# Kernel optimization log

Hardware: AMD Instinct MI355X
Metric: run time of the kernel (lower is better)

## Reference

```python
import jax, jax.numpy as jnp
import numpy as np

N, E, IN, ED, H, C = 50000, 800000, 128, 32, 4, 32
HC = H * C
SCALE = 1.0 / float(np.sqrt(C))


def _seg_softmax(t, idx, n):
    # t: [E, H], idx: [E] target-node ids -> per-segment softmax over incoming edges
    m = jax.ops.segment_max(t, idx, num_segments=n)
    m = jnp.where(jnp.isfinite(m), m, 0.0)
    e = jnp.exp(t - m[idx])
    z = jax.ops.segment_sum(e, idx, num_segments=n)
    return e / (z[idx] + 1e-16)


def setup_inputs() -> dict:
    key = jax.random.key(0)
    ks = jax.random.split(key, 26)
    w = lambda k, shape: (jax.random.normal(k, shape, jnp.float32) * 0.05)
    return {
        "x": jax.random.normal(ks[0], (N, IN), jnp.float32),
        "edge_index": jax.random.randint(ks[1], (2, E), 0, N),
        "edge_attr": jax.random.normal(ks[2], (E, ED), jnp.float32),
        # DifferentialGraphAttention params (dual QK groups + lambda)
        "Wq1": w(ks[3], (HC, IN)), "Wq2": w(ks[4], (HC, IN)),
        "Wk1": w(ks[5], (HC, IN)), "Wk2": w(ks[6], (HC, IN)),
        "Wvd": w(ks[7], (HC, IN)),
        "Wkr1": w(ks[8], (HC, ED)), "Wkr2": w(ks[9], (HC, ED)),
        "Wvrd": w(ks[10], (HC, ED)),
        "Woutd": w(ks[11], (HC, HC)),
        "lam": jnp.float32(0.8),
        # RelationActivationAttention params
        "Wqa": w(ks[12], (HC, IN)), "Wka": w(ks[13], (HC, IN)), "Wva": w(ks[14], (HC, IN)),
        "Wkra": w(ks[15], (HC, ED)), "Wvra": w(ks[16], (HC, ED)),
        "Wouta": w(ks[17], (HC, HC)),
        # Hybrid fusion params
        "Wproj": w(ks[18], (HC, 2 * HC)), "bproj": jnp.zeros((HC,), jnp.float32),
        "Win": w(ks[19], (HC, IN)), "b_in": jnp.zeros((HC,), jnp.float32),
        "rms_w": jnp.ones((HC,), jnp.float32),
    }


def reference(x, edge_index, edge_attr, Wq1, Wq2, Wk1, Wk2, Wvd, Wkr1, Wkr2, Wvrd,
              Woutd, lam, Wqa, Wka, Wva, Wkra, Wvra, Wouta, Wproj, bproj, Win, b_in,
              rms_w):
    src, dst = edge_index[0], edge_index[1]

    def nproj(W):  # [N, HC] -> [N, H, C]
        return (x @ W.T).reshape(N, H, C)

    def eproj(W):  # [E, HC] -> [E, H, C]
        return (edge_attr @ W.T).reshape(E, H, C)

    # ---- differential relation aggregation branch ----
    Q1, Q2, K1, K2, Vd = nproj(Wq1), nproj(Wq2), nproj(Wk1), nproj(Wk2), nproj(Wvd)
    t1 = jnp.sum(Q1[dst] * (K1[src] + eproj(Wkr1)), axis=-1) * SCALE  # [E, H]
    t2 = jnp.sum(Q2[dst] * (K2[src] + eproj(Wkr2)), axis=-1) * SCALE
    a_diff = _seg_softmax(t1, dst, N) - lam * _seg_softmax(t2, dst, N)
    msg_d = (Vd[src] + eproj(Wvrd)) * a_diff[..., None]               # [E, H, C]
    h_aggr = jax.ops.segment_sum(msg_d, dst, num_segments=N).reshape(N, HC) @ Woutd.T

    # ---- relation activation branch ----
    Qa, Ka, Va = nproj(Wqa), nproj(Wka), nproj(Wva)
    ta = jnp.sum(Qa[dst] * (Ka[src] + eproj(Wkra)), axis=-1) * SCALE  # [E, H]
    a_act = _seg_softmax(ta, dst, N)
    msg_a = (Va[src] + eproj(Wvra)) * a_act[..., None]
    h_actv = jax.ops.segment_sum(msg_a, dst, num_segments=N).reshape(N, HC) @ Wouta.T

    # ---- hybrid fusion + residual + RMSNorm ----
    h = jnp.concatenate([h_aggr, h_actv], axis=-1) @ Wproj.T + bproj
    h = h + (x @ Win.T + b_in)
    h = h * jax.lax.rsqrt(jnp.mean(h * h, axis=-1, keepdims=True) + 1e-6) * rms_w
    return h
```

## Files before the change

### kernel.cpp

```cpp
#include <hip/hip_runtime.h>

typedef unsigned short u16;
typedef unsigned int   u32;
typedef _Float16 half8 __attribute__((ext_vector_type(8)));
typedef _Float16 half2v __attribute__((ext_vector_type(2)));
typedef float    f32x4 __attribute__((ext_vector_type(4)));

#define NN 50000
#define EE 800000
#define SCALE 0.17677669529663687f
#define NB 49

#define O_WNODET   0ul
#define O_WFT      393216ul
#define O_WF1      524288ul
#define O_WF3      589824ul
#define O_HIST     655360ul
#define O_BSUM     855360ul
#define O_BOFF     855616ul
#define O_OFF      856064ul
#define O_CUR      1056768ul
#define O_PERM     1257472ul
#define O_NODEF    7657472ul
#define O_G        161257472ul

__device__ __forceinline__ float fin(float x){
  return (x == x && fabsf(x) < 3e38f) ? x : 0.f;
}
__device__ __forceinline__ u32 packh(float a, float b){
  union{ u32 u; _Float16 h[2]; } cv; cv.h[0]=(_Float16)a; cv.h[1]=(_Float16)b; return cv.u;
}
union H2U { u32 u; half2v h; };
__device__ __forceinline__ half2v h2(u32 u){ H2U c; c.u=u; return c.h; }
__device__ __forceinline__ u32 u2(half2v h){ H2U c; c.h=h; return c.u; }

__global__ __launch_bounds__(256) void prep1(
    const float* __restrict__ Wq1, const float* __restrict__ Wq2, const float* __restrict__ Wqa,
    const float* __restrict__ Wk1, const float* __restrict__ Wk2, const float* __restrict__ Wka,
    const float* __restrict__ Wvd, const float* __restrict__ Wva, const float* __restrict__ Win,
    const float* __restrict__ Wkr1, const float* __restrict__ Wkr2, const float* __restrict__ Wkra,
    const float* __restrict__ Wproj, const float* __restrict__ Woutd, const float* __restrict__ Wouta,
    _Float16* __restrict__ WnodeT, float* __restrict__ Wf1, float* __restrict__ Wf3)
{
  int job = blockIdx.x*256 + threadIdx.x;
  if (job < 1536*128) {
    int n = job >> 7, kk = job & 127;
    int slot = n >> 7, o = n & 127;
    float val;
    if (slot==3 || slot==4 || slot==5) {
      const float* Wkr = (slot==3)?Wkr1:(slot==4)?Wkr2:Wkra;
      const float* Wq  = (slot==3)?Wq1 :(slot==4)?Wq2 :Wqa;
      int h=o>>5, j=o&31;
      float s=0.f;
      for (int c=0;c<32;c++)
        s += Wkr[(h*32+c)*32 + j] * Wq[(h*32+c)*128 + kk];
      val = s;
    } else {
      const float* W = (slot==0)?Wq1:(slot==1)?Wq2:(slot==2)?Wqa:
                       (slot==6)?Wk1:(slot==7)?Wk2:(slot==8)?Wka:
                       (slot==9)?Wvd:(slot==10)?Wva:Win;
      val = W[o*128 + kk];
    }
    WnodeT[n*128 + kk] = (_Float16)fin(val);
  } else {
    int idx = job - 1536*128;
    int which = idx >> 14;
    int r = idx & 16383;
    int o = r >> 7, v = r & 127;
    const float* Wout = which ? Wouta : Woutd;
    float s=0.f;
    for (int u=0;u<128;u++)
      s += Wproj[o*256 + which*128 + u] * Wout[u*128 + v];
    (which?Wf3:Wf1)[o*128+v] = fin(s);
  }
}

__global__ __launch_bounds__(256) void prep2(
    const float* __restrict__ Wf1, const float* __restrict__ Wf3,
    const float* __restrict__ Wvrd, const float* __restrict__ Wvra,
    _Float16* __restrict__ WfT)
{
  int job = blockIdx.x*256 + threadIdx.x;
  int o = job >> 9, kk = job & 511;
  int seg = kk >> 7, v = kk & 127;
  float val;
  if (seg==0) val = Wf1[o*128+v];
  else if (seg==2) val = Wf3[o*128+v];
  else {
    const float* Wf = (seg==1)?Wf1:Wf3;
    const float* Wv = (seg==1)?Wvrd:Wvra;
    int h=v>>5, j=v&31; float s=0.f;
    for (int c=0;c<32;c++)
      s += Wf[o*128 + h*32 + c] * Wv[(h*32+c)*32 + j];
    val = s;
  }
  WfT[o*512 + kk] = (_Float16)fin(val);
}

__global__ __launch_bounds__(256) void gemm_node(
    const float* __restrict__ x, const _Float16* __restrict__ WnodeT,
    const float* __restrict__ b_in, _Float16* __restrict__ nodeF)
{
  __shared__ _Float16 As[128][72];
  __shared__ _Float16 Bs[128][72];
  int m0 = blockIdx.x * 128;
  int n0 = blockIdx.y * 128;
  int tid = threadIdx.x;
  int lane = tid & 63, wave = tid >> 6;
  int lm = lane & 15, lq = lane >> 4;
  int mbase = wave*32;
  f32x4 acc[2][8];
  #pragma unroll
  for (int i=0;i<2;i++)
    #pragma unroll
    for (int j=0;j<8;j++) acc[i][j] = (f32x4){0.f,0.f,0.f,0.f};

  for (int kt=0; kt<2; kt++){
    int kk0 = kt*64;
    #pragma unroll
    for (int i=0;i<4;i++){
      int c = tid + i*256;
      int row = c >> 3, kc = (c & 7) * 8;
      int grow = m0 + row;
      half8 hv;
      if (grow < NN){
        float4 v0 = *(const float4*)(x + (size_t)grow*128 + kk0 + kc);
        float4 v1 = *(const float4*)(x + (size_t)grow*128 + kk0 + kc + 4);
        hv[0]=(_Float16)v0.x; hv[1]=(_Float16)v0.y; hv[2]=(_Float16)v0.z; hv[3]=(_Float16)v0.w;
        hv[4]=(_Float16)v1.x; hv[5]=(_Float16)v1.y; hv[6]=(_Float16)v1.z; hv[7]=(_Float16)v1.w;
      } else {
        #pragma unroll
        for (int j=0;j<8;j++) hv[j] = (_Float16)0.f;
      }
      *(half8*)&As[row][kc] = hv;
      *(half8*)&Bs[row][kc] = *(const half8*)(WnodeT + (size_t)(n0+row)*128 + kk0 + kc);
    }
    __syncthreads();
    #pragma unroll
    for (int ks=0; ks<64; ks+=32){
      half8 a0 = *(half8*)&As[mbase + lm][ks + lq*8];
      half8 a1 = *(half8*)&As[mbase + 16 + lm][ks + lq*8];
      #pragma unroll
      for (int ct=0; ct<8; ct++){
        half8 b = *(half8*)&Bs[ct*16 + lm][ks + lq*8];
        acc[0][ct] = __builtin_amdgcn_mfma_f32_16x16x32_f16(a0, b, acc[0][ct], 0,0,0);
        acc[1][ct] = __builtin_amdgcn_mfma_f32_16x16x32_f16(a1, b, acc[1][ct], 0,0,0);
      }
    }
    __syncthreads();
  }
  #pragma unroll
  for (int rt=0; rt<2; rt++){
    #pragma unroll
    for (int reg=0; reg<4; reg++){
      int row = m0 + mbase + rt*16 + lq*4 + reg;
      if (row < NN){
        #pragma unroll
        for (int ct=0; ct<8; ct++){
          int colg = n0 + ct*16 + lm;
          float bias = (colg >= 1408) ? b_in[colg-1408] : 0.f;
          nodeF[(size_t)row*1536 + colg] = (_Float16)fin(acc[rt][ct][reg] + bias);
        }
      }
    }
  }
}

__global__ __launch_bounds__(256) void hist_k(const int* __restrict__ ei, int* __restrict__ hist){
  int e = blockIdx.x*256 + threadIdx.x;
  int d = ei[EE + e];
  if ((unsigned)d < (unsigned)NN) atomicAdd(&hist[d], 1);
}

__global__ __launch_bounds__(1024) void scan1(const int* __restrict__ hist,
                                              int* __restrict__ loc, int* __restrict__ bsum){
  __shared__ int buf[1024];
  int i = blockIdx.x*1024 + threadIdx.x;
  int v = (i < NN) ? hist[i] : 0;
  buf[threadIdx.x] = v;
  __syncthreads();
  int xv = v;
  for (int s = 1; s < 1024; s <<= 1){
    int t = 0;
    if ((int)threadIdx.x >= s) t = buf[threadIdx.x - s];
    __syncthreads();
    xv += t;
    buf[threadIdx.x] = xv;
    __syncthreads();
  }
  if (i < NN) loc[i] = xv - v;
  if (threadIdx.x == 1023) bsum[blockIdx.x] = xv;
}

__global__ __launch_bounds__(64) void scan2(const int* __restrict__ bsum, int* __restrict__ boff){
  int t = threadIdx.x;
  int v = (t < NB) ? bsum[t] : 0;
  int x = v;
  for (int s = 1; s < 64; s <<= 1){
    int u = __shfl_up(x, s);
    if (t >= s) x += u;
  }
  if (t < NB) boff[t] = x - v;
}

__global__ __launch_bounds__(256) void scatter_k(const int* __restrict__ ei,
                                                 const int* __restrict__ loc, const int* __restrict__ boff,
                                                 int* __restrict__ cur, int2* __restrict__ pe2){
  int e = blockIdx.x*256 + threadIdx.x;
  int d = ei[EE + e];
  if ((unsigned)d >= (unsigned)NN) return;
  int pos = loc[d] + boff[d>>10] + atomicAdd(&cur[d], 1);
  if ((unsigned)pos < (unsigned)EE) pe2[pos] = make_int2(e, ei[e]);
}

__global__ __launch_bounds__(256) void attn_k(
    const int2* __restrict__ pe2, const int* __restrict__ hist,
    const int* __restrict__ loc, const int* __restrict__ boff,
    const u32* __restrict__ nf, const float4* __restrict__ ea4,
    const float* __restrict__ lamp, u32* __restrict__ G)
{
  int lane = threadIdx.x & 63, wave = threadIdx.x >> 6;
  int node = blockIdx.x*4 + wave;
  if (node >= NN) return;
  int E = lane >> 4;
  int l = lane & 15;
  int h = l >> 2;
  u32 bd = (u32)node * 768u;
  const u32* pd = nf + bd;

  H2U q1[4], q2[4], qa[4], r1[4], r2[4], ra[4];
  {
    uint4 a = *(const uint4*)(pd +        l*4);
    uint4 b = *(const uint4*)(pd +  64 + l*4);
    uint4 c = *(const uint4*)(pd + 128 + l*4);
    q1[0].u=a.x; q1[1].u=a.y; q1[2].u=a.z; q1[3].u=a.w;
    q2[0].u=b.x; q2[1].u=b.y; q2[2].u=b.z; q2[3].u=b.w;
    qa[0].u=c.x; qa[1].u=c.y; qa[2].u=c.z; qa[3].u=c.w;
    int rb = h*16 + (l&3)*4;
    uint4 d = *(const uint4*)(pd + 192 + rb);
    uint4 e = *(const uint4*)(pd + 256 + rb);
    uint4 f = *(const uint4*)(pd + 320 + rb);
    r1[0].u=d.x; r1[1].u=d.y; r1[2].u=d.z; r1[3].u=d.w;
    r2[0].u=e.x; r2[1].u=e.y; r2[2].u=e.z; r2[3].u=e.w;
    ra[0].u=f.x; ra[1].u=f.y; ra[2].u=f.z; ra[3].u=f.w;
  }

  int k = hist[node];
  if (k < 0) k = 0;
  if (k > 64) k = 64;
  int o = loc[node] + boff[node>>10];
  if (o < 0) o = 0;

  H2U s1v[4], s2v[4], sav[4], s1e[4], s2e[4], sae[4];
  #pragma unroll
  for (int t=0;t<4;t++){ s1v[t].u=0; s2v[t].u=0; sav[t].u=0; s1e[t].u=0; s2e[t].u=0; sae[t].u=0; }
  float z1=0.f, z2=0.f, za=0.f;

  int iters = (k + 3) >> 2;
  for (int it=0; it<iters; it++){
    int ei = it*4 + E;
    bool valid = ei < k;
    int ci = valid ? ei : (k-1);
    int2 es = pe2[o + ci];
    int sn = es.y; if ((unsigned)sn >= (unsigned)NN) sn = 0;
    int ee = es.x; if ((unsigned)ee >= (unsigned)EE) ee = 0;
    const u32* ps = nf + (u32)sn * 768u + (u32)(l*4);
    uint4 K1 = *(const uint4*)(ps + 384);
    uint4 K2 = *(const uint4*)(ps + 448);
    uint4 KA = *(const uint4*)(ps + 512);
    uint4 VD = *(const uint4*)(ps + 576);
    uint4 VA = *(const uint4*)(ps + 640);
    float4 ef0 = ea4[(size_t)ee*8 + (l&3)*2];
    float4 ef1 = ea4[(size_t)ee*8 + (l&3)*2 + 1];
    half2v e0 = {(_Float16)ef0.x, (_Float16)ef0.y};
    half2v e1 = {(_Float16)ef0.z, (_Float16)ef0.w};
    half2v e2 = {(_Float16)ef1.x, (_Float16)ef1.y};
    half2v e3 = {(_Float16)ef1.z, (_Float16)ef1.w};

    half2v p1h = q1[0].h*h2(K1.x) + q1[1].h*h2(K1.y) + q1[2].h*h2(K1.z) + q1[3].h*h2(K1.w)
               + r1[0].h*e0 + r1[1].h*e1 + r1[2].h*e2 + r1[3].h*e3;
    half2v p2h = q2[0].h*h2(K2.x) + q2[1].h*h2(K2.y) + q2[2].h*h2(K2.z) + q2[3].h*h2(K2.w)
               + r2[0].h*e0 + r2[1].h*e1 + r2[2].h*e2 + r2[3].h*e3;
    half2v pah = qa[0].h*h2(KA.x) + qa[1].h*h2(KA.y) + qa[2].h*h2(KA.z) + qa[3].h*h2(KA.w)
               + ra[0].h*e0 + ra[1].h*e1 + ra[2].h*e2 + ra[3].h*e3;

    H2U c1, c2, c3, t;
    c1.h = p1h; c2.h = p2h; c3.h = pah;
    t.u = __shfl_xor(c1.u, 1); c1.h += t.h;
    t.u = __shfl_xor(c2.u, 1); c2.h += t.h;
    t.u = __shfl_xor(c3.u, 1); c3.h += t.h;
    t.u = __shfl_xor(c1.u, 2); c1.h += t.h;
    t.u = __shfl_xor(c2.u, 2); c2.h += t.h;
    t.u = __shfl_xor(c3.u, 2); c3.h += t.h;
    float p1 = (float)c1.h[0] + (float)c1.h[1];
    float p2 = (float)c2.h[0] + (float)c2.h[1];
    float pa = (float)c3.h[0] + (float)c3.h[1];

    float w1 = valid ? __expf(p1*SCALE) : 0.f;
    float w2 = valid ? __expf(p2*SCALE) : 0.f;
    float wa = valid ? __expf(pa*SCALE) : 0.f;
    _Float16 w1f = (_Float16)w1, w2f = (_Float16)w2, waf = (_Float16)wa;
    half2v w1h = {w1f, w1f}, w2h = {w2f, w2f}, wah = {waf, waf};

    s1v[0].h += w1h*h2(VD.x); s1v[1].h += w1h*h2(VD.y); s1v[2].h += w1h*h2(VD.z); s1v[3].h += w1h*h2(VD.w);
    s2v[0].h += w2h*h2(VD.x); s2v[1].h += w2h*h2(VD.y); s2v[2].h += w2h*h2(VD.z); s2v[3].h += w2h*h2(VD.w);
    sav[0].h += wah*h2(VA.x); sav[1].h += wah*h2(VA.y); sav[2].h += wah*h2(VA.z); sav[3].h += wah*h2(VA.w);
    s1e[0].h += w1h*e0; s1e[1].h += w1h*e1; s1e[2].h += w1h*e2; s1e[3].h += w1h*e3;
    s2e[0].h += w2h*e0; s2e[1].h += w2h*e1; s2e[2].h += w2h*e2; s2e[3].h += w2h*e3;
    sae[0].h += wah*e0; sae[1].h += wah*e1; sae[2].h += wah*e2; sae[3].h += wah*e3;
    z1 += w1; z2 += w2; za += wa;
  }

  #pragma unroll
  for (int s=16; s<=32; s<<=1){
    H2U t;
    #pragma unroll
    for (int j=0;j<4;j++){
      t.u = __shfl_xor(s1v[j].u, s); s1v[j].h += t.h;
      t.u = __shfl_xor(s2v[j].u, s); s2v[j].h += t.h;
      t.u = __shfl_xor(sav[j].u, s); sav[j].h += t.h;
      t.u = __shfl_xor(s1e[j].u, s); s1e[j].h += t.h;
      t.u = __shfl_xor(s2e[j].u, s); s2e[j].h += t.h;
      t.u = __shfl_xor(sae[j].u, s); sae[j].h += t.h;
    }
    z1 += __shfl_xor(z1, s); z2 += __shfl_xor(z2, s); za += __shfl_xor(za, s);
  }

  if (E == 0){
    float lamv = lamp[0];
    float i1 = 1.f/(z1+1e-16f), i2 = 1.f/(z2+1e-16f), ia = 1.f/(za+1e-16f);
    u32 gb = (u32)node*256u;
    int rb = h*16 + (l&3)*4;
    #pragma unroll
    for (int t=0;t<4;t++){
      float d0 = fin((float)s1v[t].h[0]*i1 - lamv*((float)s2v[t].h[0]*i2));
      float d1 = fin((float)s1v[t].h[1]*i1 - lamv*((float)s2v[t].h[1]*i2));
      G[gb + l*4 + t] = packh(d0, d1);
      float e0v = fin((float)s1e[t].h[0]*i1 - lamv*((float)s2e[t].h[0]*i2));
      float e1v = fin((float)s1e[t].h[1]*i1 - lamv*((float)s2e[t].h[1]*i2));
      G[gb + 64 + rb + t] = packh(e0v, e1v);
      G[gb + 128 + l*4 + t] = packh(fin((float)sav[t].h[0]*ia), fin((float)sav[t].h[1]*ia));
      G[gb + 192 + rb + t] = packh(fin((float)sae[t].h[0]*ia), fin((float)sae[t].h[1]*ia));
    }
  }
}

__global__ __launch_bounds__(256) void gemm_final(
    const _Float16* __restrict__ Gf, const _Float16* __restrict__ WfT,
    const _Float16* __restrict__ nodeF,
    const float* __restrict__ bproj, const float* __restrict__ rmsw,
    float* __restrict__ out)
{
  __shared__ _Float16 As[128][72];
  __shared__ _Float16 Bs[128][72];
  __shared__ float bS[128], rS[128];
  int m0 = blockIdx.x * 128;
  int tid = threadIdx.x;
  int lane = tid & 63, wave = tid >> 6;
  int lm = lane & 15, lq = lane >> 4;
  int mbase = wave*32;
  if (tid < 128){ bS[tid] = bproj[tid]; rS[tid] = rmsw[tid]; }
  f32x4 acc[2][8];
  #pragma unroll
  for (int i=0;i<2;i++)
    #pragma unroll
    for (int j=0;j<8;j++) acc[i][j] = (f32x4){0.f,0.f,0.f,0.f};

  for (int kt=0; kt<8; kt++){
    int kk0 = kt*64;
    #pragma unroll
    for (int i=0;i<4;i++){
      int c = tid + i*256;
      int row = c >> 3, kc = (c & 7) * 8;
      int grow = m0 + row;
      half8 av;
      if (grow < NN){
        av = *(const half8*)(Gf + (size_t)grow*512 + kk0 + kc);
      } else {
        #pragma unroll
        for (int j=0;j<8;j++) av[j] = (_Float16)0.f;
      }
      *(half8*)&As[row][kc] = av;
      *(half8*)&Bs[row][kc] = *(const half8*)(WfT + (size_t)row*512 + kk0 + kc);
    }
    __syncthreads();
    #pragma unroll
    for (int ks=0; ks<64; ks+=32){
      half8 a0 = *(half8*)&As[mbase + lm][ks + lq*8];
      half8 a1 = *(half8*)&As[mbase + 16 + lm][ks + lq*8];
      #pragma unroll
      for (int ct=0; ct<8; ct++){
        half8 b = *(half8*)&Bs[ct*16 + lm][ks + lq*8];
        acc[0][ct] = __builtin_amdgcn_mfma_f32_16x16x32_f16(a0, b, acc[0][ct], 0,0,0);
        acc[1][ct] = __builtin_amdgcn_mfma_f32_16x16x32_f16(a1, b, acc[1][ct], 0,0,0);
      }
    }
    __syncthreads();
  }
  #pragma unroll
  for (int rt=0; rt<2; rt++){
    #pragma unroll
    for (int reg=0; reg<4; reg++){
      int row = m0 + mbase + rt*16 + lq*4 + reg;
      bool ok = row < NN;
      float vals[8]; float ss = 0.f;
      #pragma unroll
      for (int ct=0; ct<8; ct++){
        int col = ct*16 + lm;
        float R = ok ? (float)nodeF[(size_t)row*1536 + 1408 + col] : 0.f;
        float v = fin(acc[rt][ct][reg] + bS[col] + R);
        vals[ct] = v; ss += v*v;
      }
      #pragma unroll
      for (int sh=1; sh<16; sh<<=1) ss += __shfl_xor(ss, sh);
      float rstd = rsqrtf(ss*(1.0f/128.f) + 1e-6f);
      if (ok){
        #pragma unroll
        for (int ct=0; ct<8; ct++){
          int col = ct*16 + lm;
          out[(size_t)row*128 + col] = fin(vals[ct]*rstd*rS[col]);
        }
      }
    }
  }
}

extern "C" void kernel_launch(void* const* d_in, const int* in_sizes, int n_in,
                              void* d_out, int out_size, void* d_ws, size_t ws_size,
                              hipStream_t stream)
{
  char* w = (char*)d_ws;
  _Float16* WnodeT = (_Float16*)(w + O_WNODET);
  _Float16* WfT    = (_Float16*)(w + O_WFT);
  float*    Wf1    = (float*)(w + O_WF1);
  float*    Wf3    = (float*)(w + O_WF3);
  int*      hist   = (int*)(w + O_HIST);
  int*      bsum   = (int*)(w + O_BSUM);
  int*      boff   = (int*)(w + O_BOFF);
  int*      loc    = (int*)(w + O_OFF);
  int*      cur    = (int*)(w + O_CUR);
  int2*     pe2    = (int2*)(w + O_PERM);
  _Float16* nodeF  = (_Float16*)(w + O_NODEF);
  _Float16* Gf     = (_Float16*)(w + O_G);

  const float* x     = (const float*)d_in[0];
  const int*   ei    = (const int*)d_in[1];
  const float* ea    = (const float*)d_in[2];
  const float* Wq1   = (const float*)d_in[3];
  const float* Wq2   = (const float*)d_in[4];
  const float* Wk1   = (const float*)d_in[5];
  const float* Wk2   = (const float*)d_in[6];
  const float* Wvd   = (const float*)d_in[7];
  const float* Wkr1  = (const float*)d_in[8];
  const float* Wkr2  = (const float*)d_in[9];
  const float* Wvrd  = (const float*)d_in[10];
  const float* Woutd = (const float*)d_in[11];
  const float* lam   = (const float*)d_in[12];
  const float* Wqa   = (const float*)d_in[13];
  const float* Wka   = (const float*)d_in[14];
  const float* Wva   = (const float*)d_in[15];
  const float* Wkra  = (const float*)d_in[16];
  const float* Wvra  = (const float*)d_in[17];
  const float* Wouta = (const float*)d_in[18];
  const float* Wproj = (const float*)d_in[19];
  const float* bproj = (const float*)d_in[20];
  const float* Win   = (const float*)d_in[21];
  const float* b_in  = (const float*)d_in[22];
  const float* rmsw  = (const float*)d_in[23];

  (void)hipMemsetAsync(hist, 0, 50000*sizeof(int), stream);
  (void)hipMemsetAsync(cur,  0, 50000*sizeof(int), stream);

  prep1<<<896, 256, 0, stream>>>(Wq1,Wq2,Wqa, Wk1,Wk2,Wka, Wvd,Wva,Win,
                                 Wkr1,Wkr2,Wkra, Wproj,Woutd,Wouta,
                                 WnodeT, Wf1, Wf3);
  prep2<<<256, 256, 0, stream>>>(Wf1, Wf3, Wvrd, Wvra, WfT);
  gemm_node<<<dim3(391,12), 256, 0, stream>>>(x, WnodeT, b_in, nodeF);
  hist_k<<<3125, 256, 0, stream>>>(ei, hist);
  scan1<<<NB, 1024, 0, stream>>>(hist, loc, bsum);
  scan2<<<1, 64, 0, stream>>>(bsum, boff);
  scatter_k<<<3125, 256, 0, stream>>>(ei, loc, boff, cur, pe2);
  attn_k<<<12500, 256, 0, stream>>>(pe2, hist, loc, boff, (const u32*)nodeF,
                                    (const float4*)ea, lam, (u32*)Gf);
  gemm_final<<<391, 256, 0, stream>>>(Gf, WfT, nodeF, bproj, rmsw, (float*)d_out);
}
```

Before: 622.5 us.

## Split node features into Q and KV buffers and software-pipeline edge gathers

The node-feature matrix is split into a per-node Q/residual buffer (896 halves) and a compact K/V buffer (640 halves), so gathered source rows are contiguous and smaller. The attention edge loop now prefetches the next iteration's K/V rows, edge attributes and the edge index two steps ahead, overlapping gather latency with compute. This uses more registers, which may lower occupancy. The workspace offsets for the new buffers are also changed.

```diff
diff --git a/kernel.cpp b/kernel.cpp
--- a/kernel.cpp
+++ b/kernel.cpp
@@ -21,7 +21,8 @@
 #define O_OFF      856064ul
 #define O_CUR      1056768ul
 #define O_PERM     1257472ul
-#define O_NODEF    7657472ul
+#define O_NODEQ    7657472ul
+#define O_NODEKV   97257472ul
 #define O_G        161257472ul
 
 __device__ __forceinline__ float fin(float x){
@@ -99,12 +100,14 @@
 
 __global__ __launch_bounds__(256) void gemm_node(
     const float* __restrict__ x, const _Float16* __restrict__ WnodeT,
-    const float* __restrict__ b_in, _Float16* __restrict__ nodeF)
+    const float* __restrict__ b_in,
+    _Float16* __restrict__ nodeQ, _Float16* __restrict__ nodeKV)
 {
   __shared__ _Float16 As[128][72];
   __shared__ _Float16 Bs[128][72];
   int m0 = blockIdx.x * 128;
-  int n0 = blockIdx.y * 128;
+  int slot = blockIdx.y;
+  int n0 = slot * 128;
   int tid = threadIdx.x;
   int lane = tid & 63, wave = tid >> 6;
   int lm = lane & 15, lq = lane >> 4;
@@ -157,9 +160,15 @@
       if (row < NN){
         #pragma unroll
         for (int ct=0; ct<8; ct++){
-          int colg = n0 + ct*16 + lm;
-          float bias = (colg >= 1408) ? b_in[colg-1408] : 0.f;
-          nodeF[(size_t)row*1536 + colg] = (_Float16)fin(acc[rt][ct][reg] + bias);
+          int col = ct*16 + lm;
+          float bias = (slot == 11) ? b_in[col] : 0.f;
+          _Float16 hv = (_Float16)fin(acc[rt][ct][reg] + bias);
+          if (slot < 6)
+            nodeQ[(size_t)row*896 + slot*128 + col] = hv;
+          else if (slot < 11)
+            nodeKV[(size_t)row*640 + (slot-6)*128 + col] = hv;
+          else
+            nodeQ[(size_t)row*896 + 768 + col] = hv;
         }
       }
     }
@@ -216,7 +225,8 @@
 __global__ __launch_bounds__(256) void attn_k(
     const int2* __restrict__ pe2, const int* __restrict__ hist,
     const int* __restrict__ loc, const int* __restrict__ boff,
-    const u32* __restrict__ nf, const float4* __restrict__ ea4,
+    const u32* __restrict__ nfQ, const u32* __restrict__ nfKV,
+    const float4* __restrict__ ea4,
     const float* __restrict__ lamp, u32* __restrict__ G)
 {
   int lane = threadIdx.x & 63, wave = threadIdx.x >> 6;
@@ -224,9 +234,9 @@
   if (node >= NN) return;
   int E = lane >> 4;
   int l = lane & 15;
-  int h = l >> 2;
-  u32 bd = (u32)node * 768u;
-  const u32* pd = nf + bd;
+  int h = l >> 4 ? 0 : (l >> 2);
+  h = (l >> 2);
+  const u32* pd = nfQ + (u32)node * 448u;
 
   H2U q1[4], q2[4], qa[4], r1[4], r2[4], ra[4];
   {
@@ -257,31 +267,63 @@
   float z1=0.f, z2=0.f, za=0.f;
 
   int iters = (k + 3) >> 2;
-  for (int it=0; it<iters; it++){
-    int ei = it*4 + E;
-    bool valid = ei < k;
-    int ci = valid ? ei : (k-1);
+
+  uint4 K1c, K2c, KAc, VDc, VAc; float4 e0c, e1c;
+  int2 esn;
+
+  if (iters > 0){
+    int ci = (E < k) ? E : (k-1);
     int2 es = pe2[o + ci];
     int sn = es.y; if ((unsigned)sn >= (unsigned)NN) sn = 0;
     int ee = es.x; if ((unsigned)ee >= (unsigned)EE) ee = 0;
-    const u32* ps = nf + (u32)sn * 768u + (u32)(l*4);
-    uint4 K1 = *(const uint4*)(ps + 384);
-    uint4 K2 = *(const uint4*)(ps + 448);
-    uint4 KA = *(const uint4*)(ps + 512);
-    uint4 VD = *(const uint4*)(ps + 576);
-    uint4 VA = *(const uint4*)(ps + 640);
-    float4 ef0 = ea4[(size_t)ee*8 + (l&3)*2];
-    float4 ef1 = ea4[(size_t)ee*8 + (l&3)*2 + 1];
-    half2v e0 = {(_Float16)ef0.x, (_Float16)ef0.y};
-    half2v e1 = {(_Float16)ef0.z, (_Float16)ef0.w};
-    half2v e2 = {(_Float16)ef1.x, (_Float16)ef1.y};
-    half2v e3 = {(_Float16)ef1.z, (_Float16)ef1.w};
-
-    half2v p1h = q1[0].h*h2(K1.x) + q1[1].h*h2(K1.y) + q1[2].h*h2(K1.z) + q1[3].h*h2(K1.w)
+    const u32* ps = nfKV + (u32)sn*320u + (u32)(l*4);
+    K1c = *(const uint4*)(ps);
+    K2c = *(const uint4*)(ps + 64);
+    KAc = *(const uint4*)(ps + 128);
+    VDc = *(const uint4*)(ps + 192);
+    VAc = *(const uint4*)(ps + 256);
+    e0c = ea4[(size_t)ee*8 + (l&3)*2];
+    e1c = ea4[(size_t)ee*8 + (l&3)*2 + 1];
+    if (iters > 1){
+      int ei1 = 4 + E;
+      int ci1 = (ei1 < k) ? ei1 : (k-1);
+      esn = pe2[o + ci1];
+    }
+  }
+
+  for (int it=0; it<iters; it++){
+    bool valid = (it*4 + E) < k;
+    bool have_next = (it+1) < iters;
+
+    uint4 K1n, K2n, KAn, VDn, VAn; float4 e0n, e1n; int2 esnn;
+    if (have_next){
+      int sn = esn.y; if ((unsigned)sn >= (unsigned)NN) sn = 0;
+      int ee = esn.x; if ((unsigned)ee >= (unsigned)EE) ee = 0;
+      const u32* ps = nfKV + (u32)sn*320u + (u32)(l*4);
+      K1n = *(const uint4*)(ps);
+      K2n = *(const uint4*)(ps + 64);
+      KAn = *(const uint4*)(ps + 128);
+      VDn = *(const uint4*)(ps + 192);
+      VAn = *(const uint4*)(ps + 256);
+      e0n = ea4[(size_t)ee*8 + (l&3)*2];
+      e1n = ea4[(size_t)ee*8 + (l&3)*2 + 1];
+      if (it+2 < iters){
+        int ei2 = (it+2)*4 + E;
+        int ci2 = (ei2 < k) ? ei2 : (k-1);
+        esnn = pe2[o + ci2];
+      }
+    }
+
+    half2v e0 = {(_Float16)e0c.x, (_Float16)e0c.y};
+    half2v e1 = {(_Float16)e0c.z, (_Float16)e0c.w};
+    half2v e2 = {(_Float16)e1c.x, (_Float16)e1c.y};
+    half2v e3 = {(_Float16)e1c.z, (_Float16)e1c.w};
+
+    half2v p1h = q1[0].h*h2(K1c.x) + q1[1].h*h2(K1c.y) + q1[2].h*h2(K1c.z) + q1[3].h*h2(K1c.w)
                + r1[0].h*e0 + r1[1].h*e1 + r1[2].h*e2 + r1[3].h*e3;
-    half2v p2h = q2[0].h*h2(K2.x) + q2[1].h*h2(K2.y) + q2[2].h*h2(K2.z) + q2[3].h*h2(K2.w)
+    half2v p2h = q2[0].h*h2(K2c.x) + q2[1].h*h2(K2c.y) + q2[2].h*h2(K2c.z) + q2[3].h*h2(K2c.w)
                + r2[0].h*e0 + r2[1].h*e1 + r2[2].h*e2 + r2[3].h*e3;
-    half2v pah = qa[0].h*h2(KA.x) + qa[1].h*h2(KA.y) + qa[2].h*h2(KA.z) + qa[3].h*h2(KA.w)
+    half2v pah = qa[0].h*h2(KAc.x) + qa[1].h*h2(KAc.y) + qa[2].h*h2(KAc.z) + qa[3].h*h2(KAc.w)
                + ra[0].h*e0 + ra[1].h*e1 + ra[2].h*e2 + ra[3].h*e3;
 
     H2U c1, c2, c3, t;
@@ -302,13 +344,18 @@
     _Float16 w1f = (_Float16)w1, w2f = (_Float16)w2, waf = (_Float16)wa;
     half2v w1h = {w1f, w1f}, w2h = {w2f, w2f}, wah = {waf, waf};
 
-    s1v[0].h += w1h*h2(VD.x); s1v[1].h += w1h*h2(VD.y); s1v[2].h += w1h*h2(VD.z); s1v[3].h += w1h*h2(VD.w);
-    s2v[0].h += w2h*h2(VD.x); s2v[1].h += w2h*h2(VD.y); s2v[2].h += w2h*h2(VD.z); s2v[3].h += w2h*h2(VD.w);
-    sav[0].h += wah*h2(VA.x); sav[1].h += wah*h2(VA.y); sav[2].h += wah*h2(VA.z); sav[3].h += wah*h2(VA.w);
+    s1v[0].h += w1h*h2(VDc.x); s1v[1].h += w1h*h2(VDc.y); s1v[2].h += w1h*h2(VDc.z); s1v[3].h += w1h*h2(VDc.w);
+    s2v[0].h += w2h*h2(VDc.x); s2v[1].h += w2h*h2(VDc.y); s2v[2].h += w2h*h2(VDc.z); s2v[3].h += w2h*h2(VDc.w);
+    sav[0].h += wah*h2(VAc.x); sav[1].h += wah*h2(VAc.y); sav[2].h += wah*h2(VAc.z); sav[3].h += wah*h2(VAc.w);
     s1e[0].h += w1h*e0; s1e[1].h += w1h*e1; s1e[2].h += w1h*e2; s1e[3].h += w1h*e3;
     s2e[0].h += w2h*e0; s2e[1].h += w2h*e1; s2e[2].h += w2h*e2; s2e[3].h += w2h*e3;
     sae[0].h += wah*e0; sae[1].h += wah*e1; sae[2].h += wah*e2; sae[3].h += wah*e3;
     z1 += w1; z2 += w2; za += wa;
+
+    if (have_next){
+      K1c = K1n; K2c = K2n; KAc = KAn; VDc = VDn; VAc = VAn;
+      e0c = e0n; e1c = e1n; esn = esnn;
+    }
   }
 
   #pragma unroll
@@ -347,7 +394,7 @@
 
 __global__ __launch_bounds__(256) void gemm_final(
     const _Float16* __restrict__ Gf, const _Float16* __restrict__ WfT,
-    const _Float16* __restrict__ nodeF,
+    const _Float16* __restrict__ nodeQ,
     const float* __restrict__ bproj, const float* __restrict__ rmsw,
     float* __restrict__ out)
 {
@@ -407,7 +454,7 @@
       #pragma unroll
       for (int ct=0; ct<8; ct++){
         int col = ct*16 + lm;
-        float R = ok ? (float)nodeF[(size_t)row*1536 + 1408 + col] : 0.f;
+        float R = ok ? (float)nodeQ[(size_t)row*896 + 768 + col] : 0.f;
         float v = fin(acc[rt][ct][reg] + bS[col] + R);
         vals[ct] = v; ss += v*v;
       }
@@ -440,7 +487,8 @@
   int*      loc    = (int*)(w + O_OFF);
   int*      cur    = (int*)(w + O_CUR);
   int2*     pe2    = (int2*)(w + O_PERM);
-  _Float16* nodeF  = (_Float16*)(w + O_NODEF);
+  _Float16* nodeQ  = (_Float16*)(w + O_NODEQ);
+  _Float16* nodeKV = (_Float16*)(w + O_NODEKV);
   _Float16* Gf     = (_Float16*)(w + O_G);
 
   const float* x     = (const float*)d_in[0];
@@ -475,12 +523,12 @@
                                  Wkr1,Wkr2,Wkra, Wproj,Woutd,Wouta,
                                  WnodeT, Wf1, Wf3);
   prep2<<<256, 256, 0, stream>>>(Wf1, Wf3, Wvrd, Wvra, WfT);
-  gemm_node<<<dim3(391,12), 256, 0, stream>>>(x, WnodeT, b_in, nodeF);
+  gemm_node<<<dim3(391,12), 256, 0, stream>>>(x, WnodeT, b_in, nodeQ, nodeKV);
   hist_k<<<3125, 256, 0, stream>>>(ei, hist);
   scan1<<<NB, 1024, 0, stream>>>(hist, loc, bsum);
   scan2<<<1, 64, 0, stream>>>(bsum, boff);
   scatter_k<<<3125, 256, 0, stream>>>(ei, loc, boff, cur, pe2);
-  attn_k<<<12500, 256, 0, stream>>>(pe2, hist, loc, boff, (const u32*)nodeF,
-                                    (const float4*)ea, lam, (u32*)Gf);
-  gemm_final<<<391, 256, 0, stream>>>(Gf, WfT, nodeF, bproj, rmsw, (float*)d_out);
-}
+  attn_k<<<12500, 256, 0, stream>>>(pe2, hist, loc, boff, (const u32*)nodeQ,
+                                    (const u32*)nodeKV, (const float4*)ea, lam, (u32*)Gf);
+  gemm_final<<<391, 256, 0, stream>>>(Gf, WfT, nodeQ, bproj, rmsw, (float*)d_out);
+}
```

Result: no change. 623.9 us (+0.2%).
